# Optimization experiments

Hardware: AMD Instinct MI355X
Metric: run time of the kernel (lower is better)

Reference implementation:

```python
import jax, jax.numpy as jnp
import numpy as np

COST_CLASS, COST_BBOX, COST_GIOU = 1.0, 5.0, 2.0


def _cxcywh_to_xyxy(b):
    cx, cy, w, h = b[..., 0], b[..., 1], b[..., 2], b[..., 3]
    return jnp.stack([cx - 0.5 * w, cy - 0.5 * h, cx + 0.5 * w, cy + 0.5 * h], axis=-1)


def _generalized_box_iou(boxes1, boxes2):
    # boxes1 [N,4], boxes2 [M,4] in xyxy -> [N,M] GIoU
    area1 = (boxes1[:, 2] - boxes1[:, 0]) * (boxes1[:, 3] - boxes1[:, 1])
    area2 = (boxes2[:, 2] - boxes2[:, 0]) * (boxes2[:, 3] - boxes2[:, 1])
    lt = jnp.maximum(boxes1[:, None, :2], boxes2[None, :, :2])
    rb = jnp.minimum(boxes1[:, None, 2:], boxes2[None, :, 2:])
    wh = jnp.clip(rb - lt, 0.0)
    inter = wh[..., 0] * wh[..., 1]
    union = area1[:, None] + area2[None, :] - inter
    iou = inter / union
    lt_e = jnp.minimum(boxes1[:, None, :2], boxes2[None, :, :2])
    rb_e = jnp.maximum(boxes1[:, None, 2:], boxes2[None, :, 2:])
    wh_e = jnp.clip(rb_e - lt_e, 0.0)
    area_e = wh_e[..., 0] * wh_e[..., 1]
    return iou - (area_e - union) / area_e


def setup_inputs() -> dict:
    key = jax.random.key(0)
    k1, k2, k3, k4 = jax.random.split(key, 4)
    B, Q, NC, T = 16, 900, 92, 1600
    return {
        "class_logits": jax.random.normal(k1, (B, Q, NC), dtype=jnp.float32),
        "box_regression": jax.random.uniform(k2, (B, Q, 4), dtype=jnp.float32),
        "tgt_ids": jax.random.randint(k3, (T,), 0, NC, dtype=jnp.int64),
        "tgt_bbox": jax.random.uniform(k4, (T, 4), dtype=jnp.float32),
    }


def reference(class_logits, box_regression, tgt_ids, tgt_bbox):
    B, Q, NC = class_logits.shape
    out_prob = jax.nn.softmax(class_logits.reshape(B * Q, NC), axis=-1)  # [BQ, NC]
    out_bbox = box_regression.reshape(B * Q, 4)                          # [BQ, 4]
    cost_class = -out_prob[:, tgt_ids]                                   # [BQ, T]
    cost_bbox = jnp.sum(jnp.abs(out_bbox[:, None, :] - tgt_bbox[None, :, :]), axis=-1)  # L1 cdist
    cost_giou = -_generalized_box_iou(_cxcywh_to_xyxy(out_bbox), _cxcywh_to_xyxy(tgt_bbox))
    C = COST_BBOX * cost_bbox + COST_CLASS * cost_class + COST_GIOU * cost_giou
    return C.reshape(B, Q, -1)
```

## Files before the change

### kernel.cpp

```cpp
#include <hip/hip_runtime.h>
#include <math.h>

#define BB 16
#define QQ 900
#define NC 92
#define NCP 96
#define TT 1600
#define BQ (BB * QQ)

#define RT 4
#define RTILE 16
#define TK 5

__global__ __launch_bounds__(256)
void k_cost(const float* __restrict__ logits,
            const float* __restrict__ boxes,
            const int* __restrict__ tids,
            const float* __restrict__ tbox,
            float* __restrict__ out) {
    __shared__ float pexp[RTILE][NCP];

    const int row0 = blockIdx.x * RTILE;
    const int t0   = blockIdx.y * (TK * 64);

    #pragma unroll
    for (int it = 0; it < 3; ++it) {
        int idx = it * 512 + threadIdx.x * 2;
        int r = idx / NCP, c = idx - r * NCP;
        float2 v = make_float2(0.0f, 0.0f);
        if (c < NC) {
            float2 lv = *(const float2*)&logits[(row0 + r) * NC + c];
            v.x = __expf(lv.x);
            v.y = __expf(lv.y);
        }
        *(float2*)&pexp[r][c] = v;
    }

    const int tl   = threadIdx.x & 63;
    const int rg   = threadIdx.x >> 6;
    const int rloc = rg * RT;
    const int rbase = row0 + rloc;

    float rcx[RT], rcy[RT], rw[RT], rh[RT];
    float rx0[RT], ry0[RT], rx1[RT], ry1[RT], rar[RT];
    #pragma unroll
    for (int j = 0; j < RT; ++j) {
        float4 bb = ((const float4*)boxes)[rbase + j];
        rcx[j] = bb.x; rcy[j] = bb.y; rw[j] = bb.z; rh[j] = bb.w;
        rx0[j] = bb.x - 0.5f * bb.z; ry0[j] = bb.y - 0.5f * bb.w;
        rx1[j] = bb.x + 0.5f * bb.z; ry1[j] = bb.y + 0.5f * bb.w;
        rar[j] = bb.z * bb.w;
    }
    __syncthreads();

    float rinv[RT];
    {
        const int lr = tl >> 4;
        const int ls = tl & 15;
        float s = 0.0f;
        #pragma unroll
        for (int i = 0; i < 6; ++i) s += pexp[rloc + lr][ls * 6 + i];
        s += __shfl_xor(s, 1);
        s += __shfl_xor(s, 2);
        s += __shfl_xor(s, 4);
        s += __shfl_xor(s, 8);
        #pragma unroll
        for (int j = 0; j < RT; ++j)
            rinv[j] = __builtin_amdgcn_rcpf(__shfl(s, j * 16));
    }

    #pragma unroll
    for (int k = 0; k < TK; ++k) {
        const int t = t0 + k * 64 + tl;
        float4 tb = ((const float4*)tbox)[t];
        int    id = tids[t];
        float tx0 = tb.x - 0.5f * tb.z, ty0 = tb.y - 0.5f * tb.w;
        float tx1 = tb.x + 0.5f * tb.z, ty1 = tb.y + 0.5f * tb.w;
        float tar = tb.z * tb.w;
        #pragma unroll
        for (int j = 0; j < RT; ++j) {
            float l1 = fabsf(rcx[j] - tb.x) + fabsf(rcy[j] - tb.y)
                     + fabsf(rw[j]  - tb.z) + fabsf(rh[j]  - tb.w);
            float iwu = fminf(rx1[j], tx1) - fmaxf(rx0[j], tx0);
            float ihu = fminf(ry1[j], ty1) - fmaxf(ry0[j], ty0);
            float inter = fmaxf(iwu, 0.0f) * fmaxf(ihu, 0.0f);
            float uni = rar[j] + tar - inter;
            float ew = (rw[j] + tb.z) - iwu;
            float eh = (rh[j] + tb.w) - ihu;
            float ea = ew * eh;
            float num = fmaf(ea, inter - uni, uni * uni);
            float rden = __builtin_amdgcn_rcpf(uni * ea);
            float p = pexp[rloc + j][id];
            float c = fmaf(-p, rinv[j], 5.0f * l1);
            c = fmaf(-2.0f * num, rden, c);
            __builtin_nontemporal_store(c, &out[(rbase + j) * TT + t]);
        }
    }
}

extern "C" void kernel_launch(void* const* d_in, const int* in_sizes, int n_in,
                              void* d_out, int out_size, void* d_ws, size_t ws_size,
                              hipStream_t stream) {
    const float* logits = (const float*)d_in[0];
    const float* boxes  = (const float*)d_in[1];
    const int*   tids   = (const int*)  d_in[2];
    const float* tbox   = (const float*)d_in[3];
    float* out = (float*)d_out;

    k_cost<<<dim3(BQ / RTILE, TT / (TK * 64)), 256, 0, stream>>>(
        logits, boxes, tids, tbox, out);
}
```

Baseline: 29.51 us.

## Retile cost kernel to 8 rows per block covering all targets

Blocks now own 8 query rows and loop over all 1600 targets, instead of 16 rows and a 320-target slice. Each row's softmax exp and sum is computed once rather than once per target slice, which removes the redundant logits reads and exp work across the 5 slices. The grid becomes 1800 one-dimensional blocks, each doing a longer loop with 2 rows per thread. The trade-offs are a longer serial loop per thread, more reloads of the target data, and fewer rows held per thread.

```diff
diff --git a/kernel.cpp b/kernel.cpp
--- a/kernel.cpp
+++ b/kernel.cpp
@@ -8,9 +8,9 @@
 #define TT 1600
 #define BQ (BB * QQ)
 
-#define RT 4
-#define RTILE 16
-#define TK 5
+#define RT 2
+#define RTILE 8
+#define NK 25
 
 __global__ __launch_bounds__(256)
 void k_cost(const float* __restrict__ logits,
@@ -21,19 +21,26 @@
     __shared__ float pexp[RTILE][NCP];
 
     const int row0 = blockIdx.x * RTILE;
-    const int t0   = blockIdx.y * (TK * 64);
 
-    #pragma unroll
-    for (int it = 0; it < 3; ++it) {
-        int idx = it * 512 + threadIdx.x * 2;
+    {
+        int idx = threadIdx.x * 2;
         int r = idx / NCP, c = idx - r * NCP;
         float2 v = make_float2(0.0f, 0.0f);
         if (c < NC) {
             float2 lv = *(const float2*)&logits[(row0 + r) * NC + c];
-            v.x = __expf(lv.x);
-            v.y = __expf(lv.y);
+            v.x = __expf(lv.x); v.y = __expf(lv.y);
         }
         *(float2*)&pexp[r][c] = v;
+        if (threadIdx.x < 128) {
+            int idx2 = 512 + threadIdx.x * 2;
+            int r2 = idx2 / NCP, c2 = idx2 - r2 * NCP;
+            float2 v2 = make_float2(0.0f, 0.0f);
+            if (c2 < NC) {
+                float2 lv = *(const float2*)&logits[(row0 + r2) * NC + c2];
+                v2.x = __expf(lv.x); v2.y = __expf(lv.y);
+            }
+            *(float2*)&pexp[r2][c2] = v2;
+        }
     }
 
     const int tl   = threadIdx.x & 63;
@@ -55,23 +62,24 @@
 
     float rinv[RT];
     {
-        const int lr = tl >> 4;
-        const int ls = tl & 15;
-        float s = 0.0f;
-        #pragma unroll
-        for (int i = 0; i < 6; ++i) s += pexp[rloc + lr][ls * 6 + i];
+        const int lr = tl >> 5;
+        const int ls = tl & 31;
+        float s = pexp[rloc + lr][ls * 3]
+                + pexp[rloc + lr][ls * 3 + 1]
+                + pexp[rloc + lr][ls * 3 + 2];
         s += __shfl_xor(s, 1);
         s += __shfl_xor(s, 2);
         s += __shfl_xor(s, 4);
         s += __shfl_xor(s, 8);
-        #pragma unroll
-        for (int j = 0; j < RT; ++j)
-            rinv[j] = __builtin_amdgcn_rcpf(__shfl(s, j * 16));
+        s += __shfl_xor(s, 16);
+        rinv[0] = __builtin_amdgcn_rcpf(__shfl(s, 0));
+        rinv[1] = __builtin_amdgcn_rcpf(__shfl(s, 32));
     }
 
-    #pragma unroll
-    for (int k = 0; k < TK; ++k) {
-        const int t = t0 + k * 64 + tl;
+    float* o0 = out + rbase * TT + tl;
+    #pragma unroll 5
+    for (int k = 0; k < NK; ++k) {
+        const int t = k * 64 + tl;
         float4 tb = ((const float4*)tbox)[t];
         int    id = tids[t];
         float tx0 = tb.x - 0.5f * tb.z, ty0 = tb.y - 0.5f * tb.w;
@@ -93,7 +101,7 @@
             float p = pexp[rloc + j][id];
             float c = fmaf(-p, rinv[j], 5.0f * l1);
             c = fmaf(-2.0f * num, rden, c);
-            __builtin_nontemporal_store(c, &out[(rbase + j) * TT + t]);
+            __builtin_nontemporal_store(c, o0 + j * TT + k * 64);
         }
     }
 }
@@ -107,6 +115,6 @@
     const float* tbox   = (const float*)d_in[3];
     float* out = (float*)d_out;
 
-    k_cost<<<dim3(BQ / RTILE, TT / (TK * 64)), 256, 0, stream>>>(
+    k_cost<<<dim3(BQ / RTILE, 1), 256, 0, stream>>>(
         logits, boxes, tids, tbox, out);
 }
```

Result: slower. 30.29 us (+2.7%).
